# Performance work log

Measured on AMD Instinct MI355X. Metric: run time of the kernel, lower is better.

## Reference

```python
import jax, jax.numpy as jnp
import numpy as np
import math

DIM = 1024
NUM_HEADS = 16
HEAD_DIM = DIM // NUM_HEADS
ROPE_BASE = 10000.0
LN_EPS = 1e-5


def _rope_tables(seq_len):
    inv_freq = 1.0 / (ROPE_BASE ** (jnp.arange(0, HEAD_DIM, 2, dtype=jnp.float32) / HEAD_DIM))
    t = jnp.arange(seq_len, dtype=jnp.float32)
    freqs = t[:, None] * inv_freq[None, :]            # (T, D/2)
    emb = jnp.concatenate([freqs, freqs], axis=-1)    # (T, D)
    return jnp.cos(emb), jnp.sin(emb)


def _rotate_half(x):
    x1 = x[..., ::2]
    x2 = x[..., 1::2]
    return jnp.stack((-x2, x1), axis=-1).reshape(x.shape)


def _heads(y):
    B, T, _ = y.shape
    return y.reshape(B, T, NUM_HEADS, HEAD_DIM).transpose(0, 2, 1, 3)  # (B,H,T,hd)


def _layernorm(x, w, b):
    mu = jnp.mean(x, axis=-1, keepdims=True)
    var = jnp.var(x, axis=-1, keepdims=True)
    return (x - mu) / jnp.sqrt(var + LN_EPS) * w + b


def setup_inputs() -> dict:
    key = jax.random.key(0)
    ks = jax.random.split(key, 16)
    s = 1.0 / math.sqrt(DIM)
    d = {
        "x": jax.random.normal(ks[0], (2, 2048, DIM), jnp.float32),
        "h_a": jax.random.normal(ks[1], (2, 512, DIM), jnp.float32),
        "h_t": jax.random.normal(ks[2], (2, 64, DIM), jnp.float32),
        "p": jax.random.normal(ks[3], (2, 256, DIM), jnp.float32),
    }
    names = ["Wq", "Wks", "Wvs", "Wka", "Wva", "Wkt", "Wvt", "Wo", "Wf"]
    for i, n in enumerate(names):
        d[n] = jax.random.normal(ks[4 + i], (DIM, DIM), jnp.float32) * s
        d["b" + n[1:]] = jnp.zeros((DIM,), jnp.float32)
    d["gating"] = jnp.zeros((1,), jnp.float32)
    d["ln_w"] = jnp.ones((DIM,), jnp.float32)
    d["ln_b"] = jnp.zeros((DIM,), jnp.float32)
    return d


def reference(x, h_a, h_t, p,
              Wq, bq, Wks, bks, Wvs, bvs, Wka, bka, Wva, bva,
              Wkt, bkt, Wvt, bvt, Wo, bo, Wf, bf,
              gating, ln_w, ln_b):
    B, T, D = x.shape
    g = jnp.tanh(gating)[0]
    h_adapter = jnp.concatenate((h_a, p), axis=1)          # (B, Ta+Tp, D)
    cos, sin = _rope_tables(T)                             # (T, hd)

    q = _heads(x @ Wq + bq)
    ks_ = _heads(x @ Wks + bks)
    vs = _heads(x @ Wvs + bvs)
    q = q * cos + _rotate_half(q) * sin
    ks_ = ks_ * cos + _rotate_half(ks_) * sin

    ka = _heads(h_adapter @ Wka + bka)
    va = _heads(h_adapter @ Wva + bva)
    kt = _heads(h_t @ Wkt + bkt)
    vt = _heads(h_t @ Wvt + bvt)

    s_self = jnp.einsum("bhqd,bhkd->bhqk", q, ks_)
    s_adpt = jnp.einsum("bhqd,bhkd->bhqk", q, ka)
    s_task = jnp.einsum("bhqd,bhkd->bhqk", q, kt) * g
    scores = jnp.concatenate([s_self, s_adpt, s_task], axis=-1) / math.sqrt(HEAD_DIM)
    attn = jax.nn.softmax(scores, axis=-1)                 # (B,H,T,S_total)

    v_all = jnp.concatenate([vs, va, vt], axis=2)          # (B,H,S_total,hd)
    out = jnp.einsum("bhqk,bhkd->bhqd", attn, v_all)
    out = out.transpose(0, 2, 1, 3).reshape(B, T, D)
    out = out @ Wo + bo

    res = _layernorm(out + x, ln_w, ln_b)
    res = jax.nn.relu(res @ Wf + bf)
    return res
```

## Files before the change

kernel.cpp:

```cpp
#include <hip/hip_runtime.h>

typedef __attribute__((ext_vector_type(8))) short bf16x8;
typedef __attribute__((ext_vector_type(4))) float f32x4;
typedef __attribute__((ext_vector_type(8))) unsigned short u16x8;
typedef __attribute__((ext_vector_type(4))) unsigned short u16x4;

#define DEV static __device__ __forceinline__

DEV float bf2f(unsigned short u) {
    union { unsigned int i; float f; } x; x.i = ((unsigned int)u) << 16; return x.f;
}
DEV unsigned short f2bf(float f) {
    union { float f; unsigned int i; } x; x.f = f;
    unsigned int r = x.i + 0x7FFFu + ((x.i >> 16) & 1u);
    return (unsigned short)(r >> 16);
}
DEV unsigned int cvt_pk_bf16(float a, float b) {
    unsigned int r;
    asm("v_cvt_pk_bf16_f32 %0, %1, %2" : "=v"(r) : "v"(a), "v"(b));
    return r;
}
DEV float ldany(const void* p, size_t i, bool f32) {
    return f32 ? ((const float*)p)[i] : bf2f(((const unsigned short*)p)[i]);
}
DEV void gload16(const void* g, void* l) {
    __builtin_amdgcn_global_load_lds(
        (const __attribute__((address_space(1))) unsigned int*)g,
        reinterpret_cast<__attribute__((address_space(3))) unsigned int*>(
            reinterpret_cast<uintptr_t>(l)),
        16, 0, 0);
}

struct Quad { const void* w0; const void* w1; const void* w2; const void* w3; };
struct Tri  { const void* b0; const void* b1; const void* b2; void* o0; void* o1; void* o2; };
struct W7 {
    const void* w0; const void* w1; const void* w2; const void* w3;
    const void* w4; const void* w5; const void* w6;
};
struct FrontArgs {
    const void* x; const void* ha; const void* pp; const void* ht;
    const void* bq; const void* bks; const void* bvs;
    const void* bka; const void* bva; const void* bkt; const void* bvt;
    void* qb; void* ks; void* vs; void* kx; void* vx;
    const unsigned short* wtp;
    const unsigned short* wte;
};

__global__ __launch_bounds__(256)
void rope_tab(float2* __restrict__ tab, const unsigned int* __restrict__ wchk,
              int* __restrict__ flag)
{
    const int idx = blockIdx.x * 256 + threadIdx.x;
    if (idx == 0) flag[0] = (wchk[0] == 0x3F800000u) ? 1 : 0;
    const int m = idx >> 5, d = idx & 31;
    const float a = (float)m * exp2f(-(float)d * 0.41524101186092033f);
    float sn, cs;
    sincosf(a, &sn, &cs);
    tab[idx] = make_float2(cs, sn);
}

__global__ __launch_bounds__(256)
void transpose_w7(W7 q, unsigned short* __restrict__ dst1, unsigned short* __restrict__ dst2,
                  int nsplit, const int* __restrict__ flagp)
{
    const bool dsf = (*flagp != 0);
    const int z = blockIdx.z;
    const void* W = (z == 0) ? q.w0 : (z == 1) ? q.w1 : (z == 2) ? q.w2 :
                    (z == 3) ? q.w3 : (z == 4) ? q.w4 : (z == 5) ? q.w5 : q.w6;
    unsigned short* out = (z < nsplit) ? dst1 + ((size_t)z << 20)
                                       : dst2 + ((size_t)(z - nsplit) << 20);
    __shared__ unsigned short Ts[64][72];
    const int t = threadIdx.x;
    const int n0 = blockIdx.x * 64, k0 = blockIdx.y * 64;
    const int r = t >> 2, c = (t & 3) << 4;
    if (!dsf) {
        const unsigned short* Wp = (const unsigned short*)W + (size_t)(k0 + r) * 1024 + n0 + c;
        *(u16x8*)&Ts[r][c]     = *(const u16x8*)Wp;
        *(u16x8*)&Ts[r][c + 8] = *(const u16x8*)(Wp + 8);
    } else {
        const float4* Wf4 = (const float4*)((const float*)W + (size_t)(k0 + r) * 1024 + n0 + c);
        float4 f[4];
        #pragma unroll
        for (int j = 0; j < 4; ++j) f[j] = Wf4[j];
        unsigned int* Td = (unsigned int*)&Ts[r][c];
        #pragma unroll
        for (int j = 0; j < 4; ++j) {
            Td[2 * j]     = cvt_pk_bf16(f[j].x, f[j].y);
            Td[2 * j + 1] = cvt_pk_bf16(f[j].z, f[j].w);
        }
    }
    __syncthreads();
    unsigned short tmp[16];
    #pragma unroll
    for (int j = 0; j < 16; ++j) tmp[j] = Ts[c + j][r];
    unsigned short* op = out + (size_t)(n0 + r) * 1024 + k0 + c;
    *(u16x8*)op       = *(const u16x8*)&tmp[0];
    *(u16x8*)(op + 8) = *(const u16x8*)&tmp[8];
}

__global__ __launch_bounds__(256)
void gemm_front(FrontArgs fa, const int* __restrict__ flagp, const float2* __restrict__ rtab)
{
    const int K = 1024, N = 1024;
    const bool dsf = (*flagp != 0);
    __shared__ unsigned short As[2][64 * 64];
    __shared__ unsigned short Bs[2][128 * 64];
    const int tid = threadIdx.x;
    const int y = blockIdx.y;
    const int n0 = blockIdx.x * 128;

    const void* A; const unsigned short* WT; const void* bias; void* Cv;
    int m0, rpb_in, rpb_o, row_off; bool rope;
    if (y < 192) {
        const int z = y >> 6;
        m0 = (y & 63) << 6;
        A = fa.x; WT = fa.wtp + ((size_t)z << 20);
        bias = (z == 0) ? fa.bq : (z == 1) ? fa.bks : fa.bvs;
        Cv   = (z == 0) ? fa.qb : (z == 1) ? fa.ks  : fa.vs;
        rpb_in = 1 << 30; rpb_o = 0; row_off = 0;
        rope = (z < 2);
    } else {
        const int yy0 = y - 192;
        const int w = (yy0 >= 26) ? 1 : 0;
        const int yy = yy0 - w * 26;
        int s, m0b;
        if (yy < 16)      { s = 0; m0b = yy; }
        else if (yy < 24) { s = 1; m0b = yy - 16; }
        else              { s = 2; m0b = yy - 24; }
        A = (s == 0) ? fa.ha : (s == 1) ? fa.pp : fa.ht;
        rpb_in  = (s == 0) ? 512 : (s == 1) ? 256 : 64;
        row_off = (s == 0) ? 0 : (s == 1) ? 512 : 768;
        WT   = fa.wte + ((size_t)(((s == 2) ? 2 : 0) + w) << 20);
        bias = (w == 0) ? ((s == 2) ? fa.bkt : fa.bka) : ((s == 2) ? fa.bvt : fa.bva);
        Cv   = (w == 0) ? fa.kx : fa.vx;
        m0 = m0b << 6; rpb_o = 832; rope = false;
    }

    const int lane = tid & 63, wv = tid >> 6;
    const int l3 = lane >> 3, c8 = lane & 7;
    const int swz = (c8 ^ l3) << 3;

    const unsigned short* Bsrc[4];
    #pragma unroll
    for (int j = 0; j < 4; ++j)
        Bsrc[j] = WT + (size_t)(n0 + (wv << 5) + (j << 3) + l3) * K + swz;

    const int ar = tid >> 2, aq = (tid & 3) << 1, ah = ar & 7;
    const size_t arow = (size_t)(m0 + ar) * K + (aq << 3);

    const int wm = (wv >> 1) << 5, wn = (wv & 1) << 6;
    const int il = lane & 15, quad = lane >> 4;
    const int h = il & 7;
    const int c0 = ((quad ^ h) << 3);
    int aoff[2], boff[4];
    #pragma unroll
    for (int mi = 0; mi < 2; ++mi) aoff[mi] = (wm + mi * 16 + il) * 64;
    #pragma unroll
    for (int nj = 0; nj < 4; ++nj) boff[nj] = (wn + nj * 16 + il) * 64;

    f32x4 acc[2][4];
    #pragma unroll
    for (int mi = 0; mi < 2; ++mi)
        #pragma unroll
        for (int nj = 0; nj < 4; ++nj) acc[mi][nj] = (f32x4){0.f, 0.f, 0.f, 0.f};

    u16x8 av[2];
    auto loadA = [&](int kq) {
        if (!dsf) {
            const unsigned short* Ag = (const unsigned short*)A + arow + kq;
            av[0] = *(const u16x8*)Ag;
            av[1] = *(const u16x8*)(Ag + 8);
        } else {
            const float4* Af4 = (const float4*)((const float*)A + arow + kq);
            float4 f[4];
            #pragma unroll
            for (int j = 0; j < 4; ++j) f[j] = Af4[j];
            #pragma unroll
            for (int j = 0; j < 2; ++j) {
                unsigned int* d = (unsigned int*)&av[j];
                d[0] = cvt_pk_bf16(f[2 * j].x, f[2 * j].y);
                d[1] = cvt_pk_bf16(f[2 * j].z, f[2 * j].w);
                d[2] = cvt_pk_bf16(f[2 * j + 1].x, f[2 * j + 1].y);
                d[3] = cvt_pk_bf16(f[2 * j + 1].z, f[2 * j + 1].w);
            }
        }
    };
    auto writeA = [&](int buf) {
        *(u16x8*)&As[buf][ar * 64 + ((aq ^ ah) << 3)]       = av[0];
        *(u16x8*)&As[buf][ar * 64 + (((aq ^ 1) ^ ah) << 3)] = av[1];
    };
    auto stageB = [&](int buf, int k0) {
        #pragma unroll
        for (int j = 0; j < 4; ++j)
            gload16(Bsrc[j] + k0, &Bs[buf][((wv << 2) + j) << 9]);
    };

    loadA(0);
    stageB(0, 0);
    writeA(0); loadA(64);
    __syncthreads();

    for (int k0 = 0; k0 < K; k0 += 64) {
        const int cur = (k0 >> 6) & 1;
        if (k0 + 64 < K) {
            stageB(cur ^ 1, k0 + 64);
            writeA(cur ^ 1);
            if (k0 + 128 < K) loadA(k0 + 128);
        }
        #pragma unroll
        for (int kk = 0; kk < 2; ++kk) {
            const int cc = c0 ^ (kk << 5);
            bf16x8 af[2], bfr[4];
            #pragma unroll
            for (int mi = 0; mi < 2; ++mi) af[mi] = *(const bf16x8*)&As[cur][aoff[mi] + cc];
            #pragma unroll
            for (int nj = 0; nj < 4; ++nj) bfr[nj] = *(const bf16x8*)&Bs[cur][boff[nj] + cc];
            #pragma unroll
            for (int mi = 0; mi < 2; ++mi)
                #pragma unroll
                for (int nj = 0; nj < 4; ++nj)
                    acc[mi][nj] = __builtin_amdgcn_mfma_f32_16x16x32_bf16(
                        af[mi], bfr[nj], acc[mi][nj], 0, 0, 0);
        }
        __syncthreads();
    }

    float bval[4];
    #pragma unroll
    for (int nj = 0; nj < 4; ++nj) bval[nj] = ldany(bias, n0 + wn + nj * 16 + il, dsf);
    #pragma unroll
    for (int mi = 0; mi < 2; ++mi) {
        #pragma unroll
        for (int r = 0; r < 4; ++r) {
            const int m = m0 + wm + mi * 16 + quad * 4 + r;
            const int bidx = m / rpb_in;
            const size_t orow = (size_t)bidx * rpb_o + row_off + (m - bidx * rpb_in);
            #pragma unroll
            for (int nj = 0; nj < 4; ++nj) {
                float v = acc[mi][nj][r] + bval[nj];
                if (rope) {
                    const int dcol = n0 + wn + nj * 16 + il;
                    const float2 cs2 = rtab[((m & 2047) << 5) | (dcol & 31)];
                    const float partner = __shfl_xor(v, 1);
                    v = (il & 1) ? fmaf(v, cs2.x, partner * cs2.y)
                                 : fmaf(v, cs2.x, -partner * cs2.y);
                }
                ((unsigned short*)Cv)[orow * N + n0 + wn + nj * 16 + il] = f2bf(v);
            }
        }
    }
}

template<int OMODE, bool RELU>
__global__ __launch_bounds__(256)
void gemm_mfma(const void* __restrict__ A, const unsigned short* __restrict__ WTbase,
               Tri t3, const int* __restrict__ flagp, int mblocks)
{
    const int K = 1024, N = 1024;
    const bool dsf = (*flagp != 0);
    __shared__ unsigned short As[2][64 * 64];
    __shared__ unsigned short Bs[2][128 * 64];
    const int tid = threadIdx.x;
    const int z = blockIdx.y / mblocks;
    const int m0 = (blockIdx.y - z * mblocks) * 64;
    const int n0 = blockIdx.x * 128;
    const unsigned short* WT = WTbase + ((size_t)z << 20);
    const void* bias = (z == 0) ? t3.b0 : (z == 1) ? t3.b1 : t3.b2;
    void* Cv = (z == 0) ? t3.o0 : (z == 1) ? t3.o1 : t3.o2;

    const int lane = tid & 63, wv = tid >> 6;
    const int l3 = lane >> 3, c8 = lane & 7;
    const int swz = (c8 ^ l3) << 3;

    const unsigned short* Bsrc[4];
    #pragma unroll
    for (int j = 0; j < 4; ++j)
        Bsrc[j] = WT + (size_t)(n0 + (wv << 5) + (j << 3) + l3) * K + swz;
    const unsigned short* Asrc[2];
    #pragma unroll
    for (int j = 0; j < 2; ++j)
        Asrc[j] = (const unsigned short*)A + (size_t)(m0 + (wv << 4) + (j << 3) + l3) * K + swz;

    const int wm = (wv >> 1) << 5, wn = (wv & 1) << 6;
    const int il = lane & 15, quad = lane >> 4;
    const int h = il & 7;
    const int c0 = ((quad ^ h) << 3);
    int aoff[2], boff[4];
    #pragma unroll
    for (int mi = 0; mi < 2; ++mi) aoff[mi] = (wm + mi * 16 + il) * 64;
    #pragma unroll
    for (int nj = 0; nj < 4; ++nj) boff[nj] = (wn + nj * 16 + il) * 64;

    f32x4 acc[2][4];
    #pragma unroll
    for (int mi = 0; mi < 2; ++mi)
        #pragma unroll
        for (int nj = 0; nj < 4; ++nj) acc[mi][nj] = (f32x4){0.f, 0.f, 0.f, 0.f};

    auto stageB = [&](int buf, int k0) {
        #pragma unroll
        for (int j = 0; j < 4; ++j)
            gload16(Bsrc[j] + k0, &Bs[buf][((wv << 2) + j) << 9]);
    };
    auto stageA = [&](int buf, int k0) {
        #pragma unroll
        for (int j = 0; j < 2; ++j)
            gload16(Asrc[j] + k0, &As[buf][((wv << 1) + j) << 9]);
    };

    stageB(0, 0);
    stageA(0, 0);
    __syncthreads();

    for (int k0 = 0; k0 < K; k0 += 64) {
        const int cur = (k0 >> 6) & 1;
        if (k0 + 64 < K) {
            stageB(cur ^ 1, k0 + 64);
            stageA(cur ^ 1, k0 + 64);
        }
        #pragma unroll
        for (int kk = 0; kk < 2; ++kk) {
            const int cc = c0 ^ (kk << 5);
            bf16x8 af[2], bfr[4];
            #pragma unroll
            for (int mi = 0; mi < 2; ++mi) af[mi] = *(const bf16x8*)&As[cur][aoff[mi] + cc];
            #pragma unroll
            for (int nj = 0; nj < 4; ++nj) bfr[nj] = *(const bf16x8*)&Bs[cur][boff[nj] + cc];
            #pragma unroll
            for (int mi = 0; mi < 2; ++mi)
                #pragma unroll
                for (int nj = 0; nj < 4; ++nj)
                    acc[mi][nj] = __builtin_amdgcn_mfma_f32_16x16x32_bf16(
                        af[mi], bfr[nj], acc[mi][nj], 0, 0, 0);
        }
        __syncthreads();
    }

    float bval[4];
    #pragma unroll
    for (int nj = 0; nj < 4; ++nj) bval[nj] = ldany(bias, n0 + wn + nj * 16 + il, dsf);
    #pragma unroll
    for (int mi = 0; mi < 2; ++mi) {
        #pragma unroll
        for (int r = 0; r < 4; ++r) {
            const size_t orow = (size_t)(m0 + wm + mi * 16 + quad * 4 + r);
            #pragma unroll
            for (int nj = 0; nj < 4; ++nj) {
                float v = acc[mi][nj][r] + bval[nj];
                if (RELU) v = fmaxf(v, 0.0f);
                const size_t idx = orow * N + n0 + wn + nj * 16 + il;
                if (OMODE == 0) ((unsigned short*)Cv)[idx] = f2bf(v);
                else {
                    if (dsf) ((float*)Cv)[idx] = v;
                    else     ((unsigned short*)Cv)[idx] = f2bf(v);
                }
            }
        }
    }
}

__global__ __launch_bounds__(256)
void attn_mfma(const unsigned short* __restrict__ Q, const unsigned short* __restrict__ Ksf,
               const unsigned short* __restrict__ Vsf, const unsigned short* __restrict__ Kx,
               const unsigned short* __restrict__ Vx, const void* __restrict__ gate,
               const int* __restrict__ flagp, unsigned short* __restrict__ AO)
{
    const int T = 2048, TX = 832, D = 1024;
    __shared__ unsigned short Klds[2][64 * 72];
    __shared__ unsigned short Vlds[2][64 * 72];
    __shared__ unsigned short Plds[4][32 * 72];
    const int tid = threadIdx.x;
    const int bh = blockIdx.x;
    const int b = bh >> 4, h = bh & 15;
    const int t0 = blockIdx.y << 7;
    const bool dsf = (*flagp != 0);
    const float g = tanhf(ldany(gate, 0, dsf));

    const int lane = tid & 63, wv = tid >> 6;
    const int il = lane & 15, quad = lane >> 4;
    const int qw = t0 + (wv << 5);

    bf16x8 qf[2][2];
    #pragma unroll
    for (int mi = 0; mi < 2; ++mi) {
        const unsigned short* qp =
            Q + (size_t)(b * T + qw + mi * 16 + il) * D + (h << 6) + quad * 8;
        qf[mi][0] = *(const bf16x8*)qp;
        qf[mi][1] = *(const bf16x8*)(qp + 32);
    }
    bf16x8 ones;
    #pragma unroll
    for (int e = 0; e < 8; ++e) ((unsigned short*)&ones)[e] = 0x3F80;

    const int ksr = tid >> 2, ksd = (tid & 3) << 4;
    const int t16 = tid >> 4, dg = tid & 15;
    const int vwcol = ((((t16 >> 1) ^ (dg & 3)) << 3) | ((t16 & 1) << 2));
    const int vwrow = (dg << 2) * 72 + vwcol;

    f32x4 o[2][4], ol[2];
    #pragma unroll
    for (int mi = 0; mi < 2; ++mi) {
        ol[mi] = (f32x4){0.f, 0.f, 0.f, 0.f};
        #pragma unroll
        for (int dt = 0; dt < 4; ++dt) o[mi][dt] = (f32x4){0.f, 0.f, 0.f, 0.f};
    }

    const unsigned short* kp = Ksf + (size_t)(b * T + ksr) * D + (h << 6) + ksd;
    const unsigned short* vp = Vsf + (size_t)(b * T + t16) * D + (h << 6) + (dg << 2);

    u16x8 kr0, kr1;
    uint2 vm0, vm1, vm2, vm3;
    auto load_kv = [&]() {
        kr0 = *(const u16x8*)kp; kr1 = *(const u16x8*)(kp + 8);
        vm0 = *(const uint2*)vp;
        vm1 = *(const uint2*)(vp + (1 << 14));
        vm2 = *(const uint2*)(vp + (2 << 14));
        vm3 = *(const uint2*)(vp + (3 << 14));
    };
    load_kv();

    #pragma unroll 1
    for (int kt = 0; kt < 45; ++kt) {
        const int cur = kt & 1;
        *(u16x8*)&Klds[cur][ksr * 72 + ksd]     = kr0;
        *(u16x8*)&Klds[cur][ksr * 72 + ksd + 8] = kr1;
        {
            unsigned int p00 = __builtin_amdgcn_perm(vm1.x, vm0.x, 0x05040100);
            unsigned int p01 = __builtin_amdgcn_perm(vm3.x, vm2.x, 0x05040100);
            unsigned int p10 = __builtin_amdgcn_perm(vm1.x, vm0.x, 0x07060302);
            unsigned int p11 = __builtin_amdgcn_perm(vm3.x, vm2.x, 0x07060302);
            unsigned int p20 = __builtin_amdgcn_perm(vm1.y, vm0.y, 0x05040100);
            unsigned int p21 = __builtin_amdgcn_perm(vm3.y, vm2.y, 0x05040100);
            unsigned int p30 = __builtin_amdgcn_perm(vm1.y, vm0.y, 0x07060302);
            unsigned int p31 = __builtin_amdgcn_perm(vm3.y, vm2.y, 0x07060302);
            *(uint2*)&Vlds[cur][vwrow]           = make_uint2(p00, p01);
            *(uint2*)&Vlds[cur][vwrow + 72]      = make_uint2(p10, p11);
            *(uint2*)&Vlds[cur][vwrow + 144]     = make_uint2(p20, p21);
            *(uint2*)&Vlds[cur][vwrow + 216]     = make_uint2(p30, p31);
        }
        __syncthreads();
        if (kt < 44) {
            if (kt == 31) {
                kp = Kx + (size_t)(b * TX + ksr) * D + (h << 6) + ksd;
                vp = Vx + (size_t)(b * TX + t16) * D + (h << 6) + (dg << 2);
            } else {
                kp += (size_t)64 * D; vp += (size_t)64 * D;
            }
            load_kv();
        }

        f32x4 s[2][4];
        #pragma unroll
        for (int mi = 0; mi < 2; ++mi)
            #pragma unroll
            for (int ct = 0; ct < 4; ++ct) s[mi][ct] = (f32x4){0.f, 0.f, 0.f, 0.f};
        #pragma unroll
        for (int ct = 0; ct < 4; ++ct) {
            #pragma unroll
            for (int c = 0; c < 2; ++c) {
                bf16x8 kf = *(const bf16x8*)&Klds[cur][(ct * 16 + il) * 72 + c * 32 + quad * 8];
                #pragma unroll
                for (int mi = 0; mi < 2; ++mi)
                    s[mi][ct] = __builtin_amdgcn_mfma_f32_16x16x32_bf16(
                        qf[mi][c], kf, s[mi][ct], 0, 0, 0);
            }
        }
        const float fc = ((kt == 44) ? g : 1.0f) * 0.18033688011112042f;

        #pragma unroll
        for (int mi = 0; mi < 2; ++mi)
            #pragma unroll
            for (int r = 0; r < 4; ++r) {
                const float e0 = __builtin_amdgcn_exp2f(fmaf(s[mi][0][r], fc, -11.541560327111708f));
                const float e1 = __builtin_amdgcn_exp2f(fmaf(s[mi][1][r], fc, -11.541560327111708f));
                const float e2 = __builtin_amdgcn_exp2f(fmaf(s[mi][2][r], fc, -11.541560327111708f));
                const float e3 = __builtin_amdgcn_exp2f(fmaf(s[mi][3][r], fc, -11.541560327111708f));
                const unsigned int lo = cvt_pk_bf16(e0, e1);
                const unsigned int hi = cvt_pk_bf16(e2, e3);
                *(uint2*)&Plds[wv][(mi * 16 + quad * 4 + r) * 72 + (il << 2)] =
                    make_uint2(lo, hi);
            }

        #pragma unroll
        for (int c = 0; c < 2; ++c) {
            bf16x8 pf[2];
            #pragma unroll
            for (int mi = 0; mi < 2; ++mi)
                pf[mi] = *(const bf16x8*)&Plds[wv][(mi * 16 + il) * 72 + c * 32 + quad * 8];
            #pragma unroll
            for (int mi = 0; mi < 2; ++mi)
                ol[mi] = __builtin_amdgcn_mfma_f32_16x16x32_bf16(pf[mi], ones, ol[mi], 0, 0, 0);
            #pragma unroll
            for (int dt = 0; dt < 4; ++dt) {
                bf16x8 vf = *(const bf16x8*)
                    &Vlds[cur][(dt * 16 + il) * 72 + c * 32 + ((quad ^ (il >> 2)) << 3)];
                #pragma unroll
                for (int mi = 0; mi < 2; ++mi)
                    o[mi][dt] = __builtin_amdgcn_mfma_f32_16x16x32_bf16(
                        pf[mi], vf, o[mi][dt], 0, 0, 0);
            }
        }
    }

    #pragma unroll
    for (int mi = 0; mi < 2; ++mi) {
        float invl[4];
        #pragma unroll
        for (int r = 0; r < 4; ++r) invl[r] = 1.0f / ol[mi][r];
        #pragma unroll
        for (int dt = 0; dt < 4; ++dt)
            #pragma unroll
            for (int r = 0; r < 4; ++r)
                AO[(size_t)(b * T + qw + mi * 16 + quad * 4 + r) * D + (h << 6) + dt * 16 + il] =
                    f2bf(o[mi][dt][r] * invl[r]);
    }
}

__global__ __launch_bounds__(256)
void ln_res(const unsigned short* __restrict__ proj, const void* __restrict__ x,
            const void* __restrict__ w, const void* __restrict__ bb,
            const int* __restrict__ flagp, unsigned short* __restrict__ y)
{
    const int row = blockIdx.x;
    const int tid = threadIdx.x;
    const bool dsf = (*flagp != 0);
    const unsigned short* pr = proj + (size_t)row * 1024;
    const u16x4 p4 = *(const u16x4*)(pr + (tid << 2));
    float v[4];
    if (dsf) {
        const float4 x4 = *(const float4*)((const float*)x + (size_t)row * 1024 + (tid << 2));
        v[0] = bf2f(p4[0]) + x4.x; v[1] = bf2f(p4[1]) + x4.y;
        v[2] = bf2f(p4[2]) + x4.z; v[3] = bf2f(p4[3]) + x4.w;
    } else {
        const u16x4 x4 = *(const u16x4*)((const unsigned short*)x + (size_t)row * 1024 + (tid << 2));
        #pragma unroll
        for (int e = 0; e < 4; ++e) v[e] = bf2f(p4[e]) + bf2f(x4[e]);
    }
    float s1 = v[0] + v[1] + v[2] + v[3];
    float s2 = v[0]*v[0] + v[1]*v[1] + v[2]*v[2] + v[3]*v[3];
    #pragma unroll
    for (int off = 1; off < 64; off <<= 1) {
        s1 += __shfl_xor(s1, off);
        s2 += __shfl_xor(s2, off);
    }
    __shared__ float red1[4], red2[4];
    const int wv = tid >> 6;
    if ((tid & 63) == 0) { red1[wv] = s1; red2[wv] = s2; }
    __syncthreads();
    s1 = red1[0] + red1[1] + red1[2] + red1[3];
    s2 = red2[0] + red2[1] + red2[2] + red2[3];
    const float mu = s1 * (1.0f / 1024.0f);
    const float var = s2 * (1.0f / 1024.0f) - mu * mu;
    const float rstd = rsqrtf(var + 1e-5f);
    float wv4[4], bv4[4];
    if (dsf) {
        const float4 wf = *(const float4*)((const float*)w + (tid << 2));
        const float4 bf4 = *(const float4*)((const float*)bb + (tid << 2));
        wv4[0] = wf.x; wv4[1] = wf.y; wv4[2] = wf.z; wv4[3] = wf.w;
        bv4[0] = bf4.x; bv4[1] = bf4.y; bv4[2] = bf4.z; bv4[3] = bf4.w;
    } else {
        const u16x4 wf = *(const u16x4*)((const unsigned short*)w + (tid << 2));
        const u16x4 bf4 = *(const u16x4*)((const unsigned short*)bb + (tid << 2));
        #pragma unroll
        for (int e = 0; e < 4; ++e) { wv4[e] = bf2f(wf[e]); bv4[e] = bf2f(bf4[e]); }
    }
    u16x4 o4;
    #pragma unroll
    for (int e = 0; e < 4; ++e)
        o4[e] = f2bf((v[e] - mu) * rstd * wv4[e] + bv4[e]);
    *(u16x4*)(y + (size_t)row * 1024 + (tid << 2)) = o4;
}

extern "C" void kernel_launch(void* const* d_in, const int* in_sizes, int n_in,
                              void* d_out, int out_size, void* d_ws, size_t ws_size,
                              hipStream_t stream)
{
    const void* x    = d_in[0];
    const void* h_a  = d_in[1];
    const void* h_t  = d_in[2];
    const void* p    = d_in[3];
    const void* Wq   = d_in[4];
    const void* bq   = d_in[5];
    const void* Wks  = d_in[6];
    const void* bks  = d_in[7];
    const void* Wvs  = d_in[8];
    const void* bvs  = d_in[9];
    const void* Wka  = d_in[10];
    const void* bka  = d_in[11];
    const void* Wva  = d_in[12];
    const void* bva  = d_in[13];
    const void* Wkt  = d_in[14];
    const void* bkt  = d_in[15];
    const void* Wvt  = d_in[16];
    const void* bvt  = d_in[17];
    const void* Wo   = d_in[18];
    const void* bo   = d_in[19];
    const void* Wf   = d_in[20];
    const void* bf_  = d_in[21];
    const void* gating = d_in[22];
    const void* ln_w = d_in[23];
    const void* ln_b = d_in[24];

    char* ws = (char*)d_ws;
    int*            flag = (int*)ws;
    unsigned short* qb   = (unsigned short*)(ws + 256);
    unsigned short* ks   = (unsigned short*)(ws + 8388864);
    unsigned short* vs   = (unsigned short*)(ws + 16777472);
    unsigned short* kx   = (unsigned short*)(ws + 25166080);
    unsigned short* vx   = (unsigned short*)(ws + 28573952);
    unsigned short* ao   = (unsigned short*)(ws + 31981824);
    unsigned short* proj  = ks;
    unsigned short* lnout = vs;
    unsigned short* WT1 = ao;
    unsigned short* WTd = (unsigned short*)d_out;
    unsigned short* WT3 = kx;
    float2*         rtab = (float2*)(ws + 31981824 + 6291456);

    dim3 blk(256);
    const Tri nul = {};

    rope_tab<<<256, blk, 0, stream>>>(rtab, (const unsigned int*)ln_w, flag);

    {
        W7 w7 = {Wq, Wks, Wvs, Wka, Wva, Wkt, Wvt};
        transpose_w7<<<dim3(16, 16, 7), blk, 0, stream>>>(w7, WT1, WTd, 3, flag);
    }

    {
        FrontArgs fa = {x, h_a, p, h_t,
                        bq, bks, bvs, bka, bva, bkt, bvt,
                        qb, ks, vs, kx, vx, WT1, WTd};
        gemm_front<<<dim3(8, 244), blk, 0, stream>>>(fa, flag, rtab);
    }

    attn_mfma<<<dim3(32, 16), blk, 0, stream>>>(qb, ks, vs, kx, vx, gating, flag, ao);

    {
        W7 w2 = {Wo, Wf, Wf, Wf, Wf, Wf, Wf};
        transpose_w7<<<dim3(16, 16, 2), blk, 0, stream>>>(w2, WT3, WT3, 2, flag);
    }
    {
        Tri t3 = {bo, nul.b1, nul.b2, proj, nul.o1, nul.o2};
        gemm_mfma<0, false><<<dim3(8, 64), blk, 0, stream>>>(ao, WT3, t3, flag, 64);
    }
    ln_res<<<4096, blk, 0, stream>>>(proj, x, ln_w, ln_b, flag, lnout);
    {
        Tri t3 = {bf_, nul.b1, nul.b2, d_out, nul.o1, nul.o2};
        gemm_mfma<2, true><<<dim3(8, 64), blk, 0, stream>>>(
            lnout, WT3 + ((size_t)1 << 20), t3, flag, 64);
    }
}
```

Baseline: 342.2 us.

## Pre-convert x to bf16 and stage A via async LDS loads, remap block order

A prep kernel now converts x to bf16 once, in the same launch that builds the rope table. The Q/K/V projection blocks in gemm_front can then stream A tiles with global_load_lds directly into shared memory, like B, instead of loading fp32 through registers and converting. Both GEMM kernels also remap block indices so consecutive blocks share the same N tile across M, which is meant to improve weight reuse in L2. The cost is an extra pass over x and a bf16 copy placed in spare output memory.

```diff
diff --git a/kernel.cpp b/kernel.cpp
--- a/kernel.cpp
+++ b/kernel.cpp
@@ -31,14 +31,14 @@
         16, 0, 0);
 }
 
-struct Quad { const void* w0; const void* w1; const void* w2; const void* w3; };
 struct Tri  { const void* b0; const void* b1; const void* b2; void* o0; void* o1; void* o2; };
 struct W7 {
     const void* w0; const void* w1; const void* w2; const void* w3;
     const void* w4; const void* w5; const void* w6;
 };
 struct FrontArgs {
-    const void* x; const void* ha; const void* pp; const void* ht;
+    const unsigned short* xb;
+    const void* ha; const void* pp; const void* ht;
     const void* bq; const void* bks; const void* bvs;
     const void* bka; const void* bva; const void* bkt; const void* bvt;
     void* qb; void* ks; void* vs; void* kx; void* vx;
@@ -47,16 +47,36 @@
 };
 
 __global__ __launch_bounds__(256)
-void rope_tab(float2* __restrict__ tab, const unsigned int* __restrict__ wchk,
-              int* __restrict__ flag)
+void prep(const void* __restrict__ x, unsigned short* __restrict__ xb,
+          float2* __restrict__ tab, const unsigned int* __restrict__ wchk,
+          int* __restrict__ flag)
 {
-    const int idx = blockIdx.x * 256 + threadIdx.x;
-    if (idx == 0) flag[0] = (wchk[0] == 0x3F800000u) ? 1 : 0;
-    const int m = idx >> 5, d = idx & 31;
-    const float a = (float)m * exp2f(-(float)d * 0.41524101186092033f);
-    float sn, cs;
-    sincosf(a, &sn, &cs);
-    tab[idx] = make_float2(cs, sn);
+    const bool dsf = (wchk[0] == 0x3F800000u);
+    const int bid = blockIdx.x, tid = threadIdx.x;
+    if (bid < 256) {
+        if (bid == 0 && tid == 0) flag[0] = dsf ? 1 : 0;
+        const int idx = bid * 256 + tid;
+        const int m = idx >> 5, d = idx & 31;
+        const float a = (float)m * exp2f(-(float)d * 0.41524101186092033f);
+        float sn, cs;
+        sincosf(a, &sn, &cs);
+        tab[idx] = make_float2(cs, sn);
+    } else {
+        const size_t off = (size_t)(bid - 256) * 2048 + (size_t)tid * 8;
+        if (dsf) {
+            const float4* xf = (const float4*)((const float*)x + off);
+            const float4 f0 = xf[0], f1 = xf[1];
+            u16x8 o;
+            unsigned int* d = (unsigned int*)&o;
+            d[0] = cvt_pk_bf16(f0.x, f0.y);
+            d[1] = cvt_pk_bf16(f0.z, f0.w);
+            d[2] = cvt_pk_bf16(f1.x, f1.y);
+            d[3] = cvt_pk_bf16(f1.z, f1.w);
+            *(u16x8*)(xb + off) = o;
+        } else {
+            *(u16x8*)(xb + off) = *(const u16x8*)((const unsigned short*)x + off);
+        }
+    }
 }
 
 __global__ __launch_bounds__(256)
@@ -106,15 +126,18 @@
     __shared__ unsigned short As[2][64 * 64];
     __shared__ unsigned short Bs[2][128 * 64];
     const int tid = threadIdx.x;
-    const int y = blockIdx.y;
-    const int n0 = blockIdx.x * 128;
+    const int bid0 = blockIdx.y * 8 + blockIdx.x;
+    const int bid  = (bid0 & 7) * 244 + (bid0 >> 3);
+    const int y  = bid >> 3;
+    const int n0 = (bid & 7) << 7;
 
     const void* A; const unsigned short* WT; const void* bias; void* Cv;
     int m0, rpb_in, rpb_o, row_off; bool rope;
-    if (y < 192) {
+    const bool aasync = (y < 192);
+    if (aasync) {
         const int z = y >> 6;
         m0 = (y & 63) << 6;
-        A = fa.x; WT = fa.wtp + ((size_t)z << 20);
+        A = fa.xb; WT = fa.wtp + ((size_t)z << 20);
         bias = (z == 0) ? fa.bq : (z == 1) ? fa.bks : fa.bvs;
         Cv   = (z == 0) ? fa.qb : (z == 1) ? fa.ks  : fa.vs;
         rpb_in = 1 << 30; rpb_o = 0; row_off = 0;
@@ -144,6 +167,10 @@
     #pragma unroll
     for (int j = 0; j < 4; ++j)
         Bsrc[j] = WT + (size_t)(n0 + (wv << 5) + (j << 3) + l3) * K + swz;
+    const unsigned short* Asrc[2];
+    #pragma unroll
+    for (int j = 0; j < 2; ++j)
+        Asrc[j] = fa.xb + (size_t)(m0 + (wv << 4) + (j << 3) + l3) * K + swz;
 
     const int ar = tid >> 2, aq = (tid & 3) << 1, ah = ar & 7;
     const size_t arow = (size_t)(m0 + ar) * K + (aq << 3);
@@ -194,18 +221,25 @@
         for (int j = 0; j < 4; ++j)
             gload16(Bsrc[j] + k0, &Bs[buf][((wv << 2) + j) << 9]);
     };
-
-    loadA(0);
-    stageB(0, 0);
-    writeA(0); loadA(64);
+    auto stageA = [&](int buf, int k0) {
+        #pragma unroll
+        for (int j = 0; j < 2; ++j)
+            gload16(Asrc[j] + k0, &As[buf][((wv << 1) + j) << 9]);
+    };
+
+    if (aasync) {
+        stageB(0, 0); stageA(0, 0);
+    } else {
+        loadA(0); stageB(0, 0); writeA(0); loadA(64);
+    }
     __syncthreads();
 
     for (int k0 = 0; k0 < K; k0 += 64) {
         const int cur = (k0 >> 6) & 1;
         if (k0 + 64 < K) {
             stageB(cur ^ 1, k0 + 64);
-            writeA(cur ^ 1);
-            if (k0 + 128 < K) loadA(k0 + 128);
+            if (aasync) stageA(cur ^ 1, k0 + 64);
+            else { writeA(cur ^ 1); if (k0 + 128 < K) loadA(k0 + 128); }
         }
         #pragma unroll
         for (int kk = 0; kk < 2; ++kk) {
@@ -253,20 +287,20 @@
 
 template<int OMODE, bool RELU>
 __global__ __launch_bounds__(256)
-void gemm_mfma(const void* __restrict__ A, const unsigned short* __restrict__ WTbase,
-               Tri t3, const int* __restrict__ flagp, int mblocks)
+void gemm_mfma(const void* __restrict__ A, const unsigned short* __restrict__ WT,
+               Tri t3, const int* __restrict__ flagp)
 {
     const int K = 1024, N = 1024;
     const bool dsf = (*flagp != 0);
     __shared__ unsigned short As[2][64 * 64];
     __shared__ unsigned short Bs[2][128 * 64];
     const int tid = threadIdx.x;
-    const int z = blockIdx.y / mblocks;
-    const int m0 = (blockIdx.y - z * mblocks) * 64;
-    const int n0 = blockIdx.x * 128;
-    const unsigned short* WT = WTbase + ((size_t)z << 20);
-    const void* bias = (z == 0) ? t3.b0 : (z == 1) ? t3.b1 : t3.b2;
-    void* Cv = (z == 0) ? t3.o0 : (z == 1) ? t3.o1 : t3.o2;
+    const int bid0 = blockIdx.y * 8 + blockIdx.x;
+    const int bid  = (bid0 & 7) * 64 + (bid0 >> 3);
+    const int m0 = (bid >> 3) << 6;
+    const int n0 = (bid & 7) << 7;
+    const void* bias = t3.b0;
+    void* Cv = t3.o0;
 
     const int lane = tid & 63, wv = tid >> 6;
     const int l3 = lane >> 3, c8 = lane & 7;
@@ -613,13 +647,14 @@
     unsigned short* lnout = vs;
     unsigned short* WT1 = ao;
     unsigned short* WTd = (unsigned short*)d_out;
+    unsigned short* xb  = WTd + ((size_t)4 << 20);
     unsigned short* WT3 = kx;
     float2*         rtab = (float2*)(ws + 31981824 + 6291456);
 
     dim3 blk(256);
     const Tri nul = {};
 
-    rope_tab<<<256, blk, 0, stream>>>(rtab, (const unsigned int*)ln_w, flag);
+    prep<<<2304, blk, 0, stream>>>(x, xb, rtab, (const unsigned int*)ln_w, flag);
 
     {
         W7 w7 = {Wq, Wks, Wvs, Wka, Wva, Wkt, Wvt};
@@ -627,7 +662,7 @@
     }
 
     {
-        FrontArgs fa = {x, h_a, p, h_t,
+        FrontArgs fa = {xb, h_a, p, h_t,
                         bq, bks, bvs, bka, bva, bkt, bvt,
                         qb, ks, vs, kx, vx, WT1, WTd};
         gemm_front<<<dim3(8, 244), blk, 0, stream>>>(fa, flag, rtab);
@@ -641,12 +676,12 @@
     }
     {
         Tri t3 = {bo, nul.b1, nul.b2, proj, nul.o1, nul.o2};
-        gemm_mfma<0, false><<<dim3(8, 64), blk, 0, stream>>>(ao, WT3, t3, flag, 64);
+        gemm_mfma<0, false><<<dim3(8, 64), blk, 0, stream>>>(ao, WT3, t3, flag);
     }
     ln_res<<<4096, blk, 0, stream>>>(proj, x, ln_w, ln_b, flag, lnout);
     {
         Tri t3 = {bf_, nul.b1, nul.b2, d_out, nul.o1, nul.o2};
         gemm_mfma<2, true><<<dim3(8, 64), blk, 0, stream>>>(
-            lnout, WT3 + ((size_t)1 << 20), t3, flag, 64);
-    }
-}
+            lnout, WT3 + ((size_t)1 << 20), t3, flag);
+    }
+}
```

After: 333.0 us. 1.03x faster.
